# Performance work log

Measured on AMD Instinct MI355X. Metric: run time of the kernel, lower is better.

Reference implementation:

```python
import jax, jax.numpy as jnp
import numpy as np
from jax import lax

M, N, Q = 256, 65536, 64
LAMBDA_STAR = 0.1
LAMBDA_O = 0.1
T_ITERS = 16
PM_ITERS = 100


def setup_inputs() -> dict:
    key = jax.random.key(0)
    kx, kd = jax.random.split(key)
    X = jax.random.normal(kx, (M, N), dtype=jnp.float32)
    D = jax.random.normal(kd, (M, Q), dtype=jnp.float32)
    return {"X": X, "D": D}


def _power_method(D):
    # Largest eigenvalue of D^T D via 100-step power iteration (fixed random init).
    x0 = jax.random.normal(jax.random.key(1), (1, Q), dtype=D.dtype)

    def step(x, _):
        x = (x @ D.T) @ D          # [1,q] -> [1,m] -> [1,q]
        nm = jnp.linalg.norm(x)
        return x / nm, nm

    _, nms = lax.scan(step, x0, None, length=PM_ITERS)
    return nms[-1]


def reference(X, D):
    m, n = X.shape
    q = D.shape[1]
    alpha = _power_method(D)
    eta = 1.0 / alpha

    Iq = jnp.eye(q, dtype=D.dtype)
    Im = jnp.eye(m, dtype=D.dtype)
    top = jnp.concatenate([D.T @ D + LAMBDA_STAR * Iq, D.T], axis=1)   # [q, q+m]
    bot = jnp.concatenate([D, (1.0 + LAMBDA_STAR) * Im], axis=1)       # [m, q+m]
    H = jnp.eye(m + q, dtype=D.dtype) - eta * jnp.concatenate([top, bot], axis=0)
    W = eta * jnp.concatenate([D.T, Im], axis=0)                        # [(m+q), m]
    t = LAMBDA_O * eta * jnp.concatenate([jnp.zeros(q, D.dtype), jnp.ones(m, D.dtype)])

    b0 = W @ X                                                           # [(m+q), n]
    Z0 = jnp.zeros((m + q, n), dtype=X.dtype)

    def ista_step(carry, _):
        Z, b = carry
        Znew = jnp.maximum(0.0, b - t[:, None])    # thresholding (ger(t, ones) == t broadcast)
        b = b + H @ (Znew - Z)
        return (Znew, b), None

    (Z, _), _ = lax.scan(ista_step, (Z0, b0), None, length=T_ITERS)
    return Z
```

## Files before the change

### kernel.cpp

```cpp
#include <hip/hip_runtime.h>


typedef __bf16 bf16x8 __attribute__((ext_vector_type(8)));
typedef float f32x4 __attribute__((ext_vector_type(4)));

#define MFMA16(a, b, c) __builtin_amdgcn_mfma_f32_16x16x32_bf16((a), (b), (c), 0, 0, 0)

#define NTOT 65536
#define NCOL 16

__device__ __forceinline__ unsigned pk2(float a, float b) {
#if __has_builtin(__builtin_amdgcn_cvt_pk_bf16_f32)
  return __builtin_bit_cast(unsigned, __builtin_amdgcn_cvt_pk_bf16_f32(a, b));
#else
  unsigned short ua = __builtin_bit_cast(unsigned short, (__bf16)a);
  unsigned short ub = __builtin_bit_cast(unsigned short, (__bf16)b);
  return (unsigned)ua | ((unsigned)ub << 16);
#endif
}
__device__ __forceinline__ f32x4 f4(float s) { f32x4 v = {s, s, s, s}; return v; }
__device__ __forceinline__ f32x4 pfma4(f32x4 a, f32x4 b, f32x4 c) {
  return __builtin_elementwise_fma(a, b, c);
}
__device__ __forceinline__ f32x4 pmax04(f32x4 a) {
  return __builtin_elementwise_max(a, f4(0.f));
}

#define GOF(row) ((row) * 68 + (((row) >> 3) << 2))
__global__ void rnmf_prep(const float* __restrict__ D, void* __restrict__ ws) {
  float* wsf = (float*)ws;
  __bf16* Dbf = (__bf16*)((char*)ws + 256);
  __bf16* DTbf = (__bf16*)((char*)ws + 256 + 32768);

  const int tid = threadIdx.x;

  if (blockIdx.x != 0) {
    const int bs = blockIdx.x - 1;
#pragma unroll
    for (int e = 0; e < 8; ++e) {
      int i4 = bs * 2048 + e * 256 + tid;
      float4 dv = *(const float4*)(D + i4 * 4);
      uint2 u; u.x = pk2(dv.x, dv.y); u.y = pk2(dv.z, dv.w);
      *(uint2*)(Dbf + i4 * 4) = u;
    }
    return;
  }

  __shared__ __bf16 DTl[64 * 264];
  __shared__ __bf16 gA[64 * 72];
  __shared__ __bf16 gB[64 * 72];
  __shared__ float gf[64 * 68 + 32];
  __shared__ __align__(16) float xv[64];
  __shared__ float etas;

  const int w = tid >> 6, lane = tid & 63, c = lane & 15, q4 = lane >> 4;

#pragma unroll
  for (int e = 0; e < 64; ++e) {
    int flat = e * 256 + tid;
    int k = flat >> 6, a = flat & 63;
    DTl[a * 264 + k] = (__bf16)D[k * 64 + a];
  }
  __syncthreads();
#pragma unroll
  for (int ct = 0; ct < 4; ++ct) {
    f32x4 acc = {0.f, 0.f, 0.f, 0.f};
#pragma unroll
    for (int kb = 0; kb < 8; ++kb) {
      bf16x8 a = *(const bf16x8*)&DTl[(16 * w + c) * 264 + 32 * kb + 8 * q4];
      bf16x8 b = *(const bf16x8*)&DTl[(16 * ct + c) * 264 + 32 * kb + 8 * q4];
      acc = MFMA16(a, b, acc);
    }
#pragma unroll
    for (int r = 0; r < 4; ++r)
      gA[(16 * w + 4 * q4 + r) * 72 + 16 * ct + c] = (__bf16)acc[r];
  }
  __syncthreads();
#pragma unroll
  for (int ct = 0; ct < 4; ++ct) {
    f32x4 acc = {0.f, 0.f, 0.f, 0.f};
#pragma unroll
    for (int kb = 0; kb < 2; ++kb) {
      bf16x8 a = *(const bf16x8*)&gA[(16 * w + c) * 72 + 32 * kb + 8 * q4];
      bf16x8 b = *(const bf16x8*)&gA[(16 * ct + c) * 72 + 32 * kb + 8 * q4];
      acc = MFMA16(a, b, acc);
    }
#pragma unroll
    for (int r = 0; r < 4; ++r)
      gB[(16 * w + 4 * q4 + r) * 72 + 16 * ct + c] = (__bf16)acc[r];
  }
  __syncthreads();
#pragma unroll
  for (int ct = 0; ct < 4; ++ct) {
    f32x4 acc = {0.f, 0.f, 0.f, 0.f};
#pragma unroll
    for (int kb = 0; kb < 2; ++kb) {
      bf16x8 a = *(const bf16x8*)&gB[(16 * w + c) * 72 + 32 * kb + 8 * q4];
      bf16x8 b = *(const bf16x8*)&gB[(16 * ct + c) * 72 + 32 * kb + 8 * q4];
      acc = MFMA16(a, b, acc);
    }
#pragma unroll
    for (int r = 0; r < 4; ++r)
      gA[(16 * w + 4 * q4 + r) * 72 + 16 * ct + c] = (__bf16)acc[r];
  }
  __syncthreads();
#pragma unroll
  for (int ct = 0; ct < 4; ++ct) {
    f32x4 acc = {0.f, 0.f, 0.f, 0.f};
#pragma unroll
    for (int kb = 0; kb < 2; ++kb) {
      bf16x8 a = *(const bf16x8*)&gA[(16 * w + c) * 72 + 32 * kb + 8 * q4];
      bf16x8 b = *(const bf16x8*)&gA[(16 * ct + c) * 72 + 32 * kb + 8 * q4];
      acc = MFMA16(a, b, acc);
    }
#pragma unroll
    for (int r = 0; r < 4; ++r)
      gf[GOF(16 * w + 4 * q4 + r) + 16 * ct + c] = acc[r];
  }
  __syncthreads();

  if (w == 0) {
    float td = gf[GOF(lane) + lane];
#pragma unroll
    for (int off = 32; off; off >>= 1) td += __shfl_xor(td, off, 64);
    const float tr = td;
    const float itr = 1.f / tr;
    xv[lane] = 1.f;
    float nm = 1.f;
    const int rowoff = GOF(lane);
    for (int itp = 0; itp < 28; ++itp) {
      float a0 = 0.f, a1 = 0.f, a2 = 0.f, a3 = 0.f;
#pragma unroll
      for (int k = 0; k < 64; k += 16) {
        float4 ga = *(const float4*)&gf[rowoff + k];
        float4 xa = *(const float4*)&xv[k];
        float4 gb = *(const float4*)&gf[rowoff + k + 4];
        float4 xb = *(const float4*)&xv[k + 4];
        float4 gc = *(const float4*)&gf[rowoff + k + 8];
        float4 xc = *(const float4*)&xv[k + 8];
        float4 gd = *(const float4*)&gf[rowoff + k + 12];
        float4 xd = *(const float4*)&xv[k + 12];
        a0 = fmaf(ga.x, xa.x, a0); a0 = fmaf(ga.y, xa.y, a0);
        a0 = fmaf(ga.z, xa.z, a0); a0 = fmaf(ga.w, xa.w, a0);
        a1 = fmaf(gb.x, xb.x, a1); a1 = fmaf(gb.y, xb.y, a1);
        a1 = fmaf(gb.z, xb.z, a1); a1 = fmaf(gb.w, xb.w, a1);
        a2 = fmaf(gc.x, xc.x, a2); a2 = fmaf(gc.y, xc.y, a2);
        a2 = fmaf(gc.z, xc.z, a2); a2 = fmaf(gc.w, xc.w, a2);
        a3 = fmaf(gd.x, xd.x, a3); a3 = fmaf(gd.y, xd.y, a3);
        a3 = fmaf(gd.z, xd.z, a3); a3 = fmaf(gd.w, xd.w, a3);
      }
      float acc = (a0 + a1) + (a2 + a3);
      float y = acc * itr;
      float n2 = y * y;
#pragma unroll
      for (int off = 32; off; off >>= 1) n2 += __shfl_xor(n2, off, 64);
      nm = sqrtf(n2);
      xv[lane] = y / nm;
    }
    if (lane == 0) {
      float e = 1.f / powf(nm * tr, 0.125f);
      wsf[0] = e;
      etas = e;
    }
  }
  __syncthreads();

  const float msc = -etas;
#pragma unroll
  for (int e = 0; e < 8; ++e) {
    int fi = e * 256 + tid;
    int a2 = fi >> 5;
    int k2 = (fi * 8) & 255;
    const __bf16* src = &DTl[a2 * 264 + k2];
    uint4 o;
    o.x = pk2(msc * (float)src[0], msc * (float)src[1]);
    o.y = pk2(msc * (float)src[2], msc * (float)src[3]);
    o.z = pk2(msc * (float)src[4], msc * (float)src[5]);
    o.w = pk2(msc * (float)src[6], msc * (float)src[7]);
    *(uint4*)(DTbf + fi * 8) = o;
  }
}

__global__ __launch_bounds__(256, 3) void rnmf_main(const float* __restrict__ X,
                                                    float* __restrict__ Z,
                                                    const void* __restrict__ ws) {
  const float* wsf = (const float*)ws;
  const __bf16* Dbf = (const __bf16*)((const char*)ws + 256);
  const __bf16* DTbf = (const __bf16*)((const char*)ws + 256 + 32768);

  __shared__ __align__(16) char arena[16640];
  float* xs = (float*)arena;
  char* smem = arena;

  const int tid = threadIdx.x;
  const int w = tid >> 6;
  const int lane = tid & 63;
  const int c = lane & 15;
  const int q4 = lane >> 4;
  const int q4h = q4 >> 1, q4l = q4 & 1;
  const int j0 = blockIdx.x * NCOL;

#pragma unroll
  for (int e = 0; e < 4; ++e) {
    int idx = e * 256 + tid;
    int row = idx >> 2, c4 = (idx & 3) * 4;
    float4 g = *(const float4*)(X + row * NTOT + j0 + c4);
    xs[(c4 + 0) * 260 + row] = g.x;
    xs[(c4 + 1) * 260 + row] = g.y;
    xs[(c4 + 2) * 260 + row] = g.z;
    xs[(c4 + 3) * 260 + row] = g.w;
  }

  const float eta = wsf[0];
  const f32x4 etav = f4(eta);
  const f32x4 metav = f4(-eta);
  const f32x4 cqv = f4(1.f - 0.1f * eta);
  const float tm = 0.1f * eta;

  bf16x8 d1[4][2];
#pragma unroll
  for (int rt = 0; rt < 4; ++rt)
#pragma unroll
    for (int kb = 0; kb < 2; ++kb)
      d1[rt][kb] = *(const bf16x8*)(Dbf + (64 * w + 16 * rt + c) * 64 + 32 * kb + 8 * q4);
  bf16x8 d2[8];
#pragma unroll
  for (int kb = 0; kb < 8; ++kb)
    d2[kb] = *(const bf16x8*)(DTbf + (16 * w + c) * 256 + 32 * kb + 8 * q4);

  __syncthreads();

  bf16x8 xbn[8];
#pragma unroll
  for (int kb = 0; kb < 8; ++kb) {
    const float* p = &xs[c * 260 + 32 * kb + 8 * q4];
    float4 lo = *(const float4*)p;
    float4 hi = *(const float4*)(p + 4);
    uint4 packed = {pk2(-lo.x, -lo.y), pk2(-lo.z, -lo.w), pk2(-hi.x, -hi.y), pk2(-hi.z, -hi.w)};
    xbn[kb] = __builtin_bit_cast(bf16x8, packed);
  }

  f32x4 bqt4;
  {
    f32x4 aA = {0.f, 0.f, 0.f, 0.f}, aB = {0.f, 0.f, 0.f, 0.f};
#pragma unroll
    for (int kb = 0; kb < 4; ++kb) aA = MFMA16(d2[kb], xbn[kb], aA);
#pragma unroll
    for (int kb = 4; kb < 8; ++kb) aB = MFMA16(d2[kb], xbn[kb], aB);
    bqt4 = aA + aB;
  }

  f32x4 bmt4[4];
#pragma unroll
  for (int rt = 0; rt < 4; ++rt) {
    const float* p = &xs[c * 260 + 64 * w + 16 * rt + 4 * q4];
    float4 v = *(const float4*)p;
    f32x4 x4 = {v.x, v.y, v.z, v.w};
    bmt4[rt] = pfma4(etav, x4, f4(-tm));
  }

  __syncthreads();

  f32x4 zq4 = pmax04(bqt4);
  f32x4 zm4[4];
#pragma unroll
  for (int rt = 0; rt < 4; ++rt) zm4[rt] = pmax04(bmt4[rt]);

  const int rb = lane * 16;
  const int vrd = 2048 + rb;
  const int wzq = w * 512 + q4h * 256 + c * 16 + 8 * q4l;
  const int wvb = 2048 + w * 2048 + q4h * 256 + c * 16 + 8 * q4l;

  {
    uint2 u; u.x = pk2(zq4[0], zq4[1]); u.y = pk2(zq4[2], zq4[3]);
    *(uint2*)(smem + wzq) = u;
  }

  for (int it = 0; it < 15; ++it) {
    __syncthreads();
    bf16x8 bz0 = *(const bf16x8*)(smem + rb);
    bf16x8 bz1 = *(const bf16x8*)(smem + rb + 1024);
#pragma unroll
    for (int rt = 0; rt < 4; ++rt) {
      f32x4 V = MFMA16(d1[rt][0], bz0, zm4[rt]);
      V = MFMA16(d1[rt][1], bz1, V);
      zm4[rt] = pmax04(pfma4(metav, V, pfma4(cqv, zm4[rt], bmt4[rt])));
      uint2 uu; uu.x = pk2(V[0], V[1]); uu.y = pk2(V[2], V[3]);
      *(uint2*)(smem + wvb + rt * 512) = uu;
    }
    __syncthreads();
    f32x4 aA = bqt4, aB = {0.f, 0.f, 0.f, 0.f};
#pragma unroll
    for (int kb = 0; kb < 4; ++kb) {
      bf16x8 bv = *(const bf16x8*)(smem + vrd + kb * 1024);
      aA = MFMA16(d2[kb], bv, aA);
    }
#pragma unroll
    for (int kb = 4; kb < 8; ++kb) {
      bf16x8 bv = *(const bf16x8*)(smem + vrd + kb * 1024);
      aB = MFMA16(d2[kb], bv, aB);
    }
    f32x4 s = aA + aB;
    zq4 = pmax04(pfma4(cqv, zq4, s));
    uint2 u; u.x = pk2(zq4[0], zq4[1]); u.y = pk2(zq4[2], zq4[3]);
    *(uint2*)(smem + wzq) = u;
  }

#pragma unroll
  for (int j = 0; j < 4; ++j)
    Z[(16 * w + 4 * q4 + j) * NTOT + j0 + c] = zq4[j];
#pragma unroll
  for (int rt = 0; rt < 4; ++rt)
#pragma unroll
    for (int j = 0; j < 4; ++j)
      Z[(64 + 64 * w + 16 * rt + 4 * q4 + j) * NTOT + j0 + c] = zm4[rt][j];
}

extern "C" void kernel_launch(void* const* d_in, const int* in_sizes, int n_in,
                              void* d_out, int out_size, void* d_ws, size_t ws_size,
                              hipStream_t stream) {
  const float* X = (const float*)d_in[0];
  const float* D = (const float*)d_in[1];
  float* Z = (float*)d_out;
  rnmf_prep<<<dim3(3), dim3(256), 0, stream>>>(D, d_ws);
  rnmf_main<<<dim3(NTOT / NCOL), dim3(256), 0, stream>>>(X, Z, d_ws);
}
```

Before: 215.7 us.

## Compute Zq update from old Z via precomputed Gram term, double-buffer to drop barrier

```diff
diff --git a/kernel.cpp b/kernel.cpp
--- a/kernel.cpp
+++ b/kernel.cpp
@@ -31,6 +31,7 @@
   float* wsf = (float*)ws;
   __bf16* Dbf = (__bf16*)((char*)ws + 256);
   __bf16* DTbf = (__bf16*)((char*)ws + 256 + 32768);
+  __bf16* Gbf = (__bf16*)((char*)ws + 256 + 65536);
 
   const int tid = threadIdx.x;
 
@@ -49,6 +50,7 @@
   __shared__ __bf16 DTl[64 * 264];
   __shared__ __bf16 gA[64 * 72];
   __shared__ __bf16 gB[64 * 72];
+  __shared__ __bf16 gG[64 * 72];
   __shared__ float gf[64 * 68 + 32];
   __shared__ __align__(16) float xv[64];
   __shared__ float etas;
@@ -72,8 +74,11 @@
       acc = MFMA16(a, b, acc);
     }
 #pragma unroll
-    for (int r = 0; r < 4; ++r)
-      gA[(16 * w + 4 * q4 + r) * 72 + 16 * ct + c] = (__bf16)acc[r];
+    for (int r = 0; r < 4; ++r) {
+      __bf16 gv = (__bf16)acc[r];
+      gA[(16 * w + 4 * q4 + r) * 72 + 16 * ct + c] = gv;
+      gG[(16 * w + 4 * q4 + r) * 72 + 16 * ct + c] = gv;
+    }
   }
   __syncthreads();
 #pragma unroll
@@ -179,6 +184,19 @@
     o.w = pk2(msc * (float)src[6], msc * (float)src[7]);
     *(uint4*)(DTbf + fi * 8) = o;
   }
+#pragma unroll
+  for (int e = 0; e < 2; ++e) {
+    int fi = e * 256 + tid;
+    int row = fi >> 3;
+    int c8 = (fi & 7) * 8;
+    const __bf16* src = &gG[row * 72 + c8];
+    uint4 o;
+    o.x = pk2(msc * (float)src[0], msc * (float)src[1]);
+    o.y = pk2(msc * (float)src[2], msc * (float)src[3]);
+    o.z = pk2(msc * (float)src[4], msc * (float)src[5]);
+    o.w = pk2(msc * (float)src[6], msc * (float)src[7]);
+    *(uint4*)(Gbf + row * 64 + c8) = o;
+  }
 }
 
 __global__ __launch_bounds__(256, 3) void rnmf_main(const float* __restrict__ X,
@@ -187,8 +205,9 @@
   const float* wsf = (const float*)ws;
   const __bf16* Dbf = (const __bf16*)((const char*)ws + 256);
   const __bf16* DTbf = (const __bf16*)((const char*)ws + 256 + 32768);
-
-  __shared__ __align__(16) char arena[16640];
+  const __bf16* Gbf = (const __bf16*)((const char*)ws + 256 + 65536);
+
+  __shared__ __align__(16) char arena[20480];
   float* xs = (float*)arena;
   char* smem = arena;
 
@@ -227,6 +246,10 @@
 #pragma unroll
   for (int kb = 0; kb < 8; ++kb)
     d2[kb] = *(const bf16x8*)(DTbf + (16 * w + c) * 256 + 32 * kb + 8 * q4);
+  bf16x8 gq[2];
+#pragma unroll
+  for (int kb = 0; kb < 2; ++kb)
+    gq[kb] = *(const bf16x8*)(Gbf + (16 * w + c) * 64 + 32 * kb + 8 * q4);
 
   __syncthreads();
 
@@ -267,44 +290,56 @@
   for (int rt = 0; rt < 4; ++rt) zm4[rt] = pmax04(bmt4[rt]);
 
   const int rb = lane * 16;
-  const int vrd = 2048 + rb;
   const int wzq = w * 512 + q4h * 256 + c * 16 + 8 * q4l;
-  const int wvb = 2048 + w * 2048 + q4h * 256 + c * 16 + 8 * q4l;
+  const int wzm = 2048 + w * 2048 + q4h * 256 + c * 16 + 8 * q4l;
 
   {
     uint2 u; u.x = pk2(zq4[0], zq4[1]); u.y = pk2(zq4[2], zq4[3]);
     *(uint2*)(smem + wzq) = u;
   }
-
-  for (int it = 0; it < 15; ++it) {
+#pragma unroll
+  for (int rt = 0; rt < 4; ++rt) {
+    uint2 u; u.x = pk2(zm4[rt][0], zm4[rt][1]); u.y = pk2(zm4[rt][2], zm4[rt][3]);
+    *(uint2*)(smem + wzm + rt * 512) = u;
+  }
+
+  auto ITER = [&](const int cb, const int nb) {
     __syncthreads();
-    bf16x8 bz0 = *(const bf16x8*)(smem + rb);
-    bf16x8 bz1 = *(const bf16x8*)(smem + rb + 1024);
+    bf16x8 zqf0 = *(const bf16x8*)(smem + cb + rb);
+    bf16x8 zqf1 = *(const bf16x8*)(smem + cb + 1024 + rb);
+    f32x4 aA = MFMA16(gq[0], zqf0, bqt4);
+    aA = MFMA16(gq[1], zqf1, aA);
 #pragma unroll
     for (int rt = 0; rt < 4; ++rt) {
-      f32x4 V = MFMA16(d1[rt][0], bz0, zm4[rt]);
-      V = MFMA16(d1[rt][1], bz1, V);
+      f32x4 V = MFMA16(d1[rt][0], zqf0, zm4[rt]);
+      V = MFMA16(d1[rt][1], zqf1, V);
       zm4[rt] = pmax04(pfma4(metav, V, pfma4(cqv, zm4[rt], bmt4[rt])));
-      uint2 uu; uu.x = pk2(V[0], V[1]); uu.y = pk2(V[2], V[3]);
-      *(uint2*)(smem + wvb + rt * 512) = uu;
-    }
-    __syncthreads();
-    f32x4 aA = bqt4, aB = {0.f, 0.f, 0.f, 0.f};
+      uint2 uu; uu.x = pk2(zm4[rt][0], zm4[rt][1]); uu.y = pk2(zm4[rt][2], zm4[rt][3]);
+      *(uint2*)(smem + nb + wzm + rt * 512) = uu;
+    }
+    f32x4 aB = {0.f, 0.f, 0.f, 0.f};
 #pragma unroll
     for (int kb = 0; kb < 4; ++kb) {
-      bf16x8 bv = *(const bf16x8*)(smem + vrd + kb * 1024);
-      aA = MFMA16(d2[kb], bv, aA);
+      bf16x8 zmf = *(const bf16x8*)(smem + cb + 2048 + kb * 1024 + rb);
+      aA = MFMA16(d2[kb], zmf, aA);
     }
 #pragma unroll
     for (int kb = 4; kb < 8; ++kb) {
-      bf16x8 bv = *(const bf16x8*)(smem + vrd + kb * 1024);
-      aB = MFMA16(d2[kb], bv, aB);
+      bf16x8 zmf = *(const bf16x8*)(smem + cb + 2048 + kb * 1024 + rb);
+      aB = MFMA16(d2[kb], zmf, aB);
     }
     f32x4 s = aA + aB;
     zq4 = pmax04(pfma4(cqv, zq4, s));
     uint2 u; u.x = pk2(zq4[0], zq4[1]); u.y = pk2(zq4[2], zq4[3]);
-    *(uint2*)(smem + wzq) = u;
-  }
+    *(uint2*)(smem + nb + wzq) = u;
+  };
+
+#pragma unroll 1
+  for (int it2 = 0; it2 < 7; ++it2) {
+    ITER(0, 10240);
+    ITER(10240, 0);
+  }
+  ITER(0, 10240);
 
 #pragma unroll
   for (int j = 0; j < 4; ++j)
```

New measurement: 216.4 us. About the same (+0.3%).
